# Performance work log

Hardware: AMD Instinct MI355X
Metric: run time of the kernel (lower is better)

The kernel has to match this reference:

```python
import jax, jax.numpy as jnp
import numpy as np

MAX_WAVELENGTH = 10000
BIG_NEG = -2.3819763e38


def _apply_rope(x, positions):
    """RoPE: positions [B,L] applied to x [B,L,H,D]."""
    d = x.shape[-1]
    freq_exponents = (2.0 / d) * jnp.arange(d // 2, dtype=jnp.float32)
    timescale = MAX_WAVELENGTH ** freq_exponents  # [D/2]
    radians = positions[..., None].astype(jnp.float32) / timescale  # [B,L,D/2]
    radians = radians[..., None, :]  # [B,L,1,D/2]
    sin, cos = jnp.sin(radians), jnp.cos(radians)
    x1, x2 = jnp.split(x, 2, axis=-1)
    return jnp.concatenate([x1 * cos - x2 * sin, x2 * cos + x1 * sin], axis=-1)


def setup_inputs() -> dict:
    key = jax.random.key(0)
    B, S, D, N, K, H = 2, 2048, 2048, 8, 1, 256  # batch, seq, features, q heads, kv heads, head_dim
    k1, k2, k3, k4 = jax.random.split(key, 4)
    x = jax.random.normal(k1, (B, S, D), dtype=jnp.float32)
    positions = jnp.broadcast_to(jnp.arange(S, dtype=jnp.int32), (B, S))
    attn_mask = jnp.tril(jnp.ones((S, S), dtype=bool))[None, None].repeat(B, axis=0)  # causal [B,1,S,S]
    q_w = jax.random.normal(k2, (N, D, H), dtype=jnp.float32) * (D ** -0.5)      # lecun_normal in_axis=-2
    kv_w = jax.random.normal(k3, (2, K, D, H), dtype=jnp.float32) * (D ** -0.5)
    out_w = jax.random.normal(k4, (N, H, D), dtype=jnp.float32) * (H ** -0.5)
    return {"x": x, "positions": positions, "attn_mask": attn_mask,
            "q_w": q_w, "kv_w": kv_w, "out_w": out_w}


def reference(x, positions, attn_mask, q_w, kv_w, out_w):
    B, T, D = x.shape
    N, _, H = q_w.shape
    K = kv_w.shape[1]
    G = N // K
    dtype = x.dtype

    q = jnp.einsum('btd,ndh->btnh', x, q_w)          # [B,T,N,H]
    kv = jnp.einsum('bsd,ckdh->cbskh', x, kv_w)      # [2,B,S,K,H]
    k, v = kv[0], kv[1]

    q = _apply_rope(q, positions) * (H ** -0.5)
    k = _apply_rope(k, positions)

    # prefill path: cache_size == S, so cache == k, v; idx = S
    qg = q.reshape(B, T, K, G, H)
    logits = jnp.einsum('btkgh,bskh->bkgts', qg, k,
                        preferred_element_type=jnp.float32)  # [B,K,G,T,S] fp32
    masked = jnp.where(attn_mask[:, :, None, :, :], logits, BIG_NEG)
    probs = jax.nn.softmax(masked, axis=-1).astype(dtype)
    enc = jnp.einsum('bkgts,bskh->btkgh', probs, v).reshape(B, T, N, H)
    out = jnp.einsum('btnh,nhd->btd', enc, out_w)
    return out
```

## Files before the change

### kernel.cpp

```cpp
#include <hip/hip_runtime.h>
#include <hip/hip_bf16.h>
#include <stdint.h>

#define BB 2
#define SS 2048
#define DD 2048
#define NHEAD 8
#define HH 256

typedef __bf16 bf16_t;
typedef __bf16 bf16x8 __attribute__((ext_vector_type(8)));
typedef __bf16 bf16x4v __attribute__((ext_vector_type(4)));
typedef __bf16 bf16x2v __attribute__((ext_vector_type(2)));
typedef float f32x4 __attribute__((ext_vector_type(4)));
typedef float f32x16 __attribute__((ext_vector_type(16)));
typedef unsigned int u32;

__device__ static inline void gload_lds16(const void* g, void* l) {
  __builtin_amdgcn_global_load_lds(
      (__attribute__((address_space(1))) void*)(g),
      (__attribute__((address_space(3))) void*)(l), 16, 0, 0);
}

__device__ static inline u32 pk2(float a, float b) {
  bf16x2v t = {(bf16_t)a, (bf16_t)b};
  return __builtin_bit_cast(u32, t);
}

__global__ void cvt_x_kernel(const float* __restrict__ x, bf16_t* __restrict__ xb) {
  size_t i = ((size_t)blockIdx.x * 256 + threadIdx.x) * 4;
  float4 v = *(const float4*)(x + i);
  bf16x4v o = {(bf16_t)v.x, (bf16_t)v.y, (bf16_t)v.z, (bf16_t)v.w};
  *(bf16x4v*)(xb + i) = o;
}

__global__ void transpose_cvt(const float* __restrict__ in, bf16_t* __restrict__ out,
                              int R, int C) {
  __shared__ float tile[32][33];
  int bx = blockIdx.x, by = blockIdx.y, z = blockIdx.z;
  in  += (size_t)z * R * C;
  out += (size_t)z * R * C;
  int tx = threadIdx.x & 31, ty = threadIdx.x >> 5;
#pragma unroll
  for (int k = 0; k < 4; ++k) {
    int r = by * 32 + ty + k * 8, c = bx * 32 + tx;
    tile[ty + k * 8][tx] = in[(size_t)r * C + c];
  }
  __syncthreads();
#pragma unroll
  for (int k = 0; k < 4; ++k) {
    int c = bx * 32 + ty + k * 8, r = by * 32 + tx;
    out[(size_t)c * R + r] = (bf16_t)tile[tx][ty + k * 8];
  }
}

template <int OUT_F32>
__global__ __launch_bounds__(512) void gemm3p(const bf16_t* __restrict__ A,
                                              const bf16_t* __restrict__ BT,
                                              void* __restrict__ C,
                                              int M, int Nc, int Kd) {
  __shared__ __attribute__((aligned(16))) char LDS[147456];
  char* Abuf = LDS;
  char* Bbuf = LDS + 98304;
  const int ntiles = Nc >> 7;
  int nwg = gridDim.x;
  int bid = ((nwg & 7) == 0) ? ((blockIdx.x & 7) * (nwg >> 3) + (blockIdx.x >> 3))
                             : blockIdx.x;
  int mt = bid / ntiles, ntb = bid % ntiles;
  int t = threadIdx.x, lane = t & 63, w = t >> 6;
  int wm = w >> 1, wn = w & 1;
  int l15 = lane & 15, lg = lane >> 4;
  int srow = t >> 3;
  int scolb = ((t & 7) * 16) ^ ((srow & 7) << 4);
  const bf16_t* Asrc = A + (size_t)(mt * 256 + srow) * Kd + (scolb >> 1);
  const bf16_t* Bsrc = BT + (size_t)(ntb * 128 + srow) * Kd + (scolb >> 1);
  const int nkt = Kd >> 6;
  f32x4 acc[4][4] = {};

#define STAGE_TILE(kt_)                                                      \
  {                                                                          \
    int buf_ = (kt_) % 3;                                                    \
    char* Ad_ = Abuf + buf_ * 32768 + t * 16;                                \
    char* Bd_ = Bbuf + buf_ * 16384 + t * 16;                                \
    const bf16_t* As_ = Asrc + (kt_)*64;                                     \
    const bf16_t* Bs_ = Bsrc + (kt_)*64;                                     \
    gload_lds16(As_, Ad_);                                                   \
    gload_lds16(As_ + (size_t)64 * Kd, Ad_ + 8192);                          \
    gload_lds16(As_ + (size_t)128 * Kd, Ad_ + 16384);                        \
    gload_lds16(As_ + (size_t)192 * Kd, Ad_ + 24576);                        \
    gload_lds16(Bs_, Bd_);                                                   \
    gload_lds16(Bs_ + (size_t)64 * Kd, Bd_ + 8192);                          \
  }

  STAGE_TILE(0);
  STAGE_TILE(1);
  asm volatile("s_waitcnt vmcnt(6)" ::: "memory");
  __builtin_amdgcn_s_barrier();
  asm volatile("" ::: "memory");
  for (int kt = 0; kt < nkt; ++kt) {
    if (kt + 2 < nkt) STAGE_TILE(kt + 2);
    const char* Ab = Abuf + (kt % 3) * 32768;
    const char* Bb = Bbuf + (kt % 3) * 16384;
    int swz = (l15 & 7) << 4;
#pragma unroll
    for (int ks = 0; ks < 2; ++ks) {
      bf16x8 af[4], bfr[4];
#pragma unroll
      for (int i = 0; i < 4; ++i)
        af[i] = *(const bf16x8*)(Ab + (wm * 64 + i * 16 + l15) * 128 +
                                 ((ks * 64 + lg * 16) ^ swz));
#pragma unroll
      for (int j = 0; j < 4; ++j)
        bfr[j] = *(const bf16x8*)(Bb + (wn * 64 + j * 16 + l15) * 128 +
                                  ((ks * 64 + lg * 16) ^ swz));
      __builtin_amdgcn_s_setprio(1);
#pragma unroll
      for (int i = 0; i < 4; ++i)
#pragma unroll
        for (int j = 0; j < 4; ++j)
          acc[i][j] = __builtin_amdgcn_mfma_f32_16x16x32_bf16(af[i], bfr[j], acc[i][j], 0, 0, 0);
      __builtin_amdgcn_s_setprio(0);
    }
    if (kt + 1 < nkt) {
      if (kt + 2 < nkt) {
        asm volatile("s_waitcnt vmcnt(6)" ::: "memory");
      } else {
        asm volatile("s_waitcnt vmcnt(0)" ::: "memory");
      }
      __builtin_amdgcn_s_barrier();
      asm volatile("" ::: "memory");
    }
  }
#undef STAGE_TILE
#pragma unroll
  for (int i = 0; i < 4; ++i)
#pragma unroll
    for (int j = 0; j < 4; ++j) {
      int row = mt * 256 + wm * 64 + i * 16 + lg * 4;
      int col = ntb * 128 + wn * 64 + j * 16 + l15;
#pragma unroll
      for (int v = 0; v < 4; ++v) {
        if (OUT_F32)
          ((float*)C)[(size_t)(row + v) * Nc + col] = acc[i][j][v];
        else
          ((bf16_t*)C)[(size_t)(row + v) * Nc + col] = (bf16_t)acc[i][j][v];
      }
    }
}

__global__ void rope_kernel(bf16_t* __restrict__ qkv, const int* __restrict__ positions) {
  int idx = blockIdx.x * 256 + threadIdx.x;
  const int QP = 4096 * 8 * 128;
  int i, row;
  bf16_t *p1, *p2;
  float scl;
  if (idx < QP) {
    i = idx & 127;
    int nh = (idx >> 7) & 7;
    row = idx >> 10;
    p1 = qkv + (size_t)row * 2560 + nh * 256 + i;
    p2 = p1 + 128;
    scl = 0.0625f;
  } else {
    int kk = idx - QP;
    if (kk >= 4096 * 128) return;
    i = kk & 127;
    row = kk >> 7;
    p1 = qkv + (size_t)row * 2560 + 2048 + i;
    p2 = p1 + 128;
    scl = 1.0f;
  }
  float pos = (float)positions[row];
  float ang = pos * __expf(-(float)i * (9.2103403719761836f / 128.f));
  float s = sinf(ang), c = cosf(ang);
  float x1 = (float)*p1, x2 = (float)*p2;
  *p1 = (bf16_t)((x1 * c - x2 * s) * scl);
  *p2 = (bf16_t)((x2 * c + x1 * s) * scl);
}

__global__ void vt_kernel(const bf16_t* __restrict__ qkv, bf16_t* __restrict__ vt) {
  __shared__ bf16_t tile[32][34];
  int bx = blockIdx.x;
  int by = blockIdx.y;
  int b = blockIdx.z;
  int tx = threadIdx.x & 31, ty = threadIdx.x >> 5;
#pragma unroll
  for (int k = 0; k < 4; ++k) {
    int s = bx * 32 + ty + k * 8, h = by * 32 + tx;
    tile[ty + k * 8][tx] = qkv[((size_t)(b * SS + s)) * 2560 + 2304 + h];
  }
  __syncthreads();
#pragma unroll
  for (int k = 0; k < 4; ++k) {
    int h = by * 32 + ty + k * 8, s = bx * 32 + tx;
    vt[((size_t)(b * HH + h)) * 2048 + s] = tile[tx][ty + k * 8];
  }
}

__global__ __launch_bounds__(512)
void flash_kernel(const bf16_t* __restrict__ qkv, const bf16_t* __restrict__ vtg,
                  bf16_t* __restrict__ enc, u32* __restrict__ ctr) {
  __shared__ __attribute__((aligned(16))) char LDSRAW[149504];
  char* Kl = LDSRAW;
  char* Vl = LDSRAW + 65536;
  char* Pl = LDSRAW + 131072;
  float* pmxL = (float*)(LDSRAW + 147456);
  float* scaleL = (float*)(LDSRAW + 147968);
  float* lsumL = (float*)(LDSRAW + 148480);
  u32* slot = (u32*)(LDSRAW + 148992);
  int t = threadIdx.x, lane = t & 63, w = t >> 6;
  int l31 = lane & 31, h5 = lane >> 5;
  bool isQK = (w < 4);
  int wq = isQK ? (w & 1) : ((w - 4) & 1);
  int sh = (w >> 1) & 1;
  int hh = ((w - 4) >> 1) & 1;
  int rk0 = t >> 5;
  int cbk = ((t & 31) * 16) ^ ((rk0 & 15) << 4);
  int rv0 = t >> 3;
  int cbv = ((t & 7) * 16) ^ ((rv0 & 7) << 4);

  for (;;) {
    if (t == 0) *slot = atomicAdd(ctr, 1);
    __syncthreads();
    u32 ti = *slot;
    if (ti >= 512u) break;
    int qt = 31 - (int)(ti >> 4);
    int b = (int)(ti >> 3) & 1, n = (int)ti & 7;
    const bf16_t* kbase = qkv + (size_t)(b * SS) * 2560 + 2048;
    int qmin = qt * 64 + wq * 32;
    int q_g = qmin + l31;
    bf16x8 qf[16];
    if (isQK) {
      const bf16_t* qrow = qkv + ((size_t)(b * SS + q_g)) * 2560 + n * 256 + h5 * 8;
#pragma unroll
      for (int i = 0; i < 16; ++i) qf[i] = *(const bf16x8*)(qrow + i * 16);
    }
    f32x16 accO[4] = {};
    float m_r = -1e30f, l_r = 0.f;
#pragma unroll
    for (int r = 0; r < 4; ++r)
      gload_lds16(kbase + (size_t)(rk0 + 16 * r) * 2560 + (cbk >> 1), Kl + t * 16 + r * 8192);
    __syncthreads();
    for (int kt = 0; kt <= qt + 1; ++kt) {
      int cur = kt & 1, prv = cur ^ 1;
      if (kt <= qt) {
#pragma unroll
        for (int r = 0; r < 4; ++r)
          gload_lds16(vtg + ((size_t)(b * HH + rv0 + 64 * r)) * 2048 + kt * 64 + (cbv >> 1),
                      Vl + cur * 32768 + t * 16 + r * 8192);
      }
      if (kt < qt) {
#pragma unroll
        for (int r = 0; r < 4; ++r)
          gload_lds16(kbase + (size_t)((kt + 1) * 64 + rk0 + 16 * r) * 2560 + (cbk >> 1),
                      Kl + prv * 32768 + t * 16 + r * 8192);
      }
      bool qact = isQK && (kt <= qt);
      bool act = qact && (kt * 64 + sh * 32 <= qmin + 31);
      bool pact = (!isQK) && (kt >= 1);
      f32x16 sc = {};
      float pm = -1e30f;
      if (qact) {
        if (act) {
          const char* Kc = Kl + cur * 32768;
          int krow = sh * 32 + l31;
          int kswz = (l31 & 15) << 4;
          __builtin_amdgcn_s_setprio(1);
#pragma unroll
          for (int i = 0; i < 16; ++i) {
            bf16x8 kf = *(const bf16x8*)(Kc + krow * 512 + ((i * 32 + h5 * 16) ^ kswz));
            sc = __builtin_amdgcn_mfma_f32_32x32x16_bf16(kf, qf[i], sc, 0, 0, 0);
          }
          __builtin_amdgcn_s_setprio(0);
          int smin = kt * 64 + sh * 32;
          if (smin + 31 > qmin) {
#pragma unroll
            for (int r = 0; r < 16; ++r) {
              int s_g = smin + ((r & 3) + 8 * (r >> 2) + 4 * h5);
              if (s_g > q_g) sc[r] = -1e30f;
            }
          }
          pm = sc[0];
#pragma unroll
          for (int r = 1; r < 16; ++r) pm = fmaxf(pm, sc[r]);
          pm = fmaxf(pm, __shfl_xor(pm, 32));
        }
        if (h5 == 0) pmxL[(wq * 2 + sh) * 32 + l31] = pm;
      }
      if (pact) {
        float sfac = scaleL[prv * 64 + wq * 32 + l31];
        if (__any(sfac != 1.f)) {
          float rv[16];
#pragma unroll
          for (int r = 0; r < 16; ++r) rv[r] = __shfl(sfac, (r & 3) + 8 * (r >> 2) + 4 * h5);
#pragma unroll
          for (int ht = 0; ht < 4; ++ht)
#pragma unroll
            for (int r = 0; r < 16; ++r) accO[ht][r] *= rv[r];
        }
        const char* Pw = Pl + prv * 8192 + wq * 4096;
        const char* Vc = Vl + prv * 32768;
        int pswz = (l31 & 7) << 4;
        __builtin_amdgcn_s_setprio(1);
#pragma unroll
        for (int j = 0; j < 2; ++j) {
          bf16x8 pf = *(const bf16x8*)(Pw + l31 * 128 + ((j * 32 + h5 * 16) ^ pswz));
#pragma unroll
          for (int ht = 0; ht < 4; ++ht) {
            int vrow = hh * 128 + ht * 32 + l31;
            bf16x8 vf = *(const bf16x8*)(Vc + vrow * 128 + ((j * 32 + h5 * 16) ^ pswz));
            accO[ht] = __builtin_amdgcn_mfma_f32_32x32x16_bf16(pf, vf, accO[ht], 0, 0, 0);
          }
        }
        __builtin_amdgcn_s_setprio(0);
      }
      asm volatile("s_waitcnt lgkmcnt(0)" ::: "memory");
      __builtin_amdgcn_s_barrier();
      asm volatile("" ::: "memory");
      if (qact) {
        float pmS = fmaxf(pmxL[(wq * 2) * 32 + l31], pmxL[(wq * 2 + 1) * 32 + l31]);
        float rsc = 1.f;
        if (pmS > m_r + 8.f) {
          rsc = __expf(m_r - pmS);
          m_r = pmS;
          l_r *= rsc;
        }
        if (sh == 0 && h5 == 0) scaleL[cur * 64 + wq * 32 + l31] = rsc;
        if (act) {
          float rs = 0.f;
#pragma unroll
          for (int r = 0; r < 16; ++r) {
            float p = __expf(sc[r] - m_r);
            sc[r] = p;
            rs += p;
          }
          rs += __shfl_xor(rs, 32);
          l_r += rs;
          u32 u0 = pk2(sc[0], sc[1]),  u1 = pk2(sc[2], sc[3]);
          u32 u2 = pk2(sc[4], sc[5]),  u3 = pk2(sc[6], sc[7]);
          u32 u4 = pk2(sc[8], sc[9]),  u5 = pk2(sc[10], sc[11]);
          u32 u6 = pk2(sc[12], sc[13]), u7 = pk2(sc[14], sc[15]);
          u32 x0 = __shfl_xor(u0, 32), x1 = __shfl_xor(u1, 32);
          u32 x2 = __shfl_xor(u2, 32), x3 = __shfl_xor(u3, 32);
          u32 x4 = __shfl_xor(u4, 32), x5 = __shfl_xor(u5, 32);
          u32 x6 = __shfl_xor(u6, 32), x7 = __shfl_xor(u7, 32);
          union { u32 wd[4]; bf16x8 v; } f0, f1;
          f0.wd[0] = h5 ? x2 : u0;  f0.wd[1] = h5 ? x3 : u1;
          f0.wd[2] = h5 ? u2 : x0;  f0.wd[3] = h5 ? u3 : x1;
          f1.wd[0] = h5 ? x6 : u4;  f1.wd[1] = h5 ? x7 : u5;
          f1.wd[2] = h5 ? u6 : x4;  f1.wd[3] = h5 ? u7 : x5;
          char* Pw = Pl + cur * 8192 + wq * 4096;
          int pswz = (l31 & 7) << 4;
          *(bf16x8*)(Pw + l31 * 128 + ((sh * 64 + h5 * 16) ^ pswz)) = f0.v;
          *(bf16x8*)(Pw + l31 * 128 + ((sh * 64 + 32 + h5 * 16) ^ pswz)) = f1.v;
        }
      }
      if (pact && ((kt - 1 < qt) || wq == 1)) {
        const char* Pw = Pl + prv * 8192 + wq * 4096;
        const char* Vc = Vl + prv * 32768;
        int pswz = (l31 & 7) << 4;
        __builtin_amdgcn_s_setprio(1);
#pragma unroll
        for (int j = 2; j < 4; ++j) {
          bf16x8 pf = *(const bf16x8*)(Pw + l31 * 128 + ((j * 32 + h5 * 16) ^ pswz));
#pragma unroll
          for (int ht = 0; ht < 4; ++ht) {
            int vrow = hh * 128 + ht * 32 + l31;
            bf16x8 vf = *(const bf16x8*)(Vc + vrow * 128 + ((j * 32 + h5 * 16) ^ pswz));
            accO[ht] = __builtin_amdgcn_mfma_f32_32x32x16_bf16(pf, vf, accO[ht], 0, 0, 0);
          }
        }
        __builtin_amdgcn_s_setprio(0);
      }
      __syncthreads();
    }
    if (isQK && h5 == 0) lsumL[sh * 64 + wq * 32 + l31] = l_r;
    __syncthreads();
    if (!isQK) {
      float lt = lsumL[wq * 32 + l31] + lsumL[64 + wq * 32 + l31];
      float rinv = 1.f / lt;
      float riv[16];
#pragma unroll
      for (int r = 0; r < 16; ++r) riv[r] = __shfl(rinv, (r & 3) + 8 * (r >> 2) + 4 * h5);
#pragma unroll
      for (int ht = 0; ht < 4; ++ht)
#pragma unroll
        for (int r = 0; r < 16; ++r) {
          int ql = (r & 3) + 8 * (r >> 2) + 4 * h5;
          enc[((size_t)(b * SS + qmin + ql)) * 2048 + n * 256 + hh * 128 + ht * 32 + l31] =
              (bf16_t)(accO[ht][r] * riv[r]);
        }
    }
  }
}

extern "C" void kernel_launch(void* const* d_in, const int* in_sizes, int n_in,
                              void* d_out, int out_size, void* d_ws, size_t ws_size,
                              hipStream_t stream) {
  const float* x = (const float*)d_in[0];
  const int* positions = (const int*)d_in[1];
  const float* qw = (const float*)d_in[3];
  const float* kvw = (const float*)d_in[4];
  const float* outw = (const float*)d_in[5];

  char* ws = (char*)d_ws;
  if (ws_size < (size_t)75497472) return;
  bf16_t* xb      = (bf16_t*)(ws);
  bf16_t* qkvwbt  = (bf16_t*)(ws + 16777216);
  bf16_t* outwbt  = (bf16_t*)(ws + 27262976);
  bf16_t* qkvb    = (bf16_t*)(ws + 35651584);
  bf16_t* vtg     = (bf16_t*)(ws + 56623104);
  bf16_t* encb    = (bf16_t*)(ws + 58720256);
  u32* ctr        = (u32*)(ws);

  cvt_x_kernel<<<8192, 256, 0, stream>>>(x, xb);
  transpose_cvt<<<dim3(8, 64, 8), 256, 0, stream>>>(qw, qkvwbt, 2048, 256);
  transpose_cvt<<<dim3(8, 64, 2), 256, 0, stream>>>(kvw, qkvwbt + (size_t)2048 * 2048, 2048, 256);
  transpose_cvt<<<dim3(64, 64, 1), 256, 0, stream>>>(outw, outwbt, 2048, 2048);
  gemm3p<0><<<320, 512, 0, stream>>>(xb, qkvwbt, qkvb, 4096, 2560, 2048);
  rope_kernel<<<18432, 256, 0, stream>>>(qkvb, positions);
  vt_kernel<<<dim3(64, 8, 2), 256, 0, stream>>>(qkvb, vtg);
  hipMemsetAsync(ctr, 0, 4, stream);
  flash_kernel<<<256, 512, 0, stream>>>(qkvb, vtg, encb, ctr);
  gemm3p<1><<<256, 512, 0, stream>>>(encb, outwbt, d_out, 4096, 2048, 2048);
}
```

Before: 209.0 us.

## Shrink GEMM tiles to 128x128 with 256 threads and split A/B staging

Replaces the 256x128 tile, 512-thread GEMM with a 128x128 tile using 256 threads (4 waves), doubling the grid size for both projection GEMMs. A is triple-buffered while B is double-buffered, and B is staged only one tile ahead, which cuts LDS use from 144KB to 80KB. The goal is more workgroups for better CU occupancy and load balance. The cost is lower per-block data reuse and more global traffic, and B now has less prefetch lead time.

```diff
diff --git a/kernel.cpp b/kernel.cpp
--- a/kernel.cpp
+++ b/kernel.cpp
@@ -55,13 +55,13 @@
 }
 
 template <int OUT_F32>
-__global__ __launch_bounds__(512) void gemm3p(const bf16_t* __restrict__ A,
+__global__ __launch_bounds__(256) void gemm2b(const bf16_t* __restrict__ A,
                                               const bf16_t* __restrict__ BT,
                                               void* __restrict__ C,
                                               int M, int Nc, int Kd) {
-  __shared__ __attribute__((aligned(16))) char LDS[147456];
+  __shared__ __attribute__((aligned(16))) char LDS[81920];
   char* Abuf = LDS;
-  char* Bbuf = LDS + 98304;
+  char* Bbuf = LDS + 49152;
   const int ntiles = Nc >> 7;
   int nwg = gridDim.x;
   int bid = ((nwg & 7) == 0) ? ((blockIdx.x & 7) * (nwg >> 3) + (blockIdx.x >> 3))
@@ -72,35 +72,41 @@
   int l15 = lane & 15, lg = lane >> 4;
   int srow = t >> 3;
   int scolb = ((t & 7) * 16) ^ ((srow & 7) << 4);
-  const bf16_t* Asrc = A + (size_t)(mt * 256 + srow) * Kd + (scolb >> 1);
+  const bf16_t* Asrc = A + (size_t)(mt * 128 + srow) * Kd + (scolb >> 1);
   const bf16_t* Bsrc = BT + (size_t)(ntb * 128 + srow) * Kd + (scolb >> 1);
   const int nkt = Kd >> 6;
   f32x4 acc[4][4] = {};
 
-#define STAGE_TILE(kt_)                                                      \
-  {                                                                          \
-    int buf_ = (kt_) % 3;                                                    \
-    char* Ad_ = Abuf + buf_ * 32768 + t * 16;                                \
-    char* Bd_ = Bbuf + buf_ * 16384 + t * 16;                                \
-    const bf16_t* As_ = Asrc + (kt_)*64;                                     \
-    const bf16_t* Bs_ = Bsrc + (kt_)*64;                                     \
-    gload_lds16(As_, Ad_);                                                   \
-    gload_lds16(As_ + (size_t)64 * Kd, Ad_ + 8192);                          \
-    gload_lds16(As_ + (size_t)128 * Kd, Ad_ + 16384);                        \
-    gload_lds16(As_ + (size_t)192 * Kd, Ad_ + 24576);                        \
-    gload_lds16(Bs_, Bd_);                                                   \
-    gload_lds16(Bs_ + (size_t)64 * Kd, Bd_ + 8192);                          \
-  }
-
-  STAGE_TILE(0);
-  STAGE_TILE(1);
-  asm volatile("s_waitcnt vmcnt(6)" ::: "memory");
+#define STAGE_A(kt_)                                                  \
+  {                                                                   \
+    char* d_ = Abuf + ((kt_) % 3) * 16384 + t * 16;                   \
+    const bf16_t* s_ = Asrc + (kt_)*64;                               \
+    gload_lds16(s_, d_);                                              \
+    gload_lds16(s_ + (size_t)32 * Kd, d_ + 4096);                     \
+    gload_lds16(s_ + (size_t)64 * Kd, d_ + 8192);                     \
+    gload_lds16(s_ + (size_t)96 * Kd, d_ + 12288);                    \
+  }
+#define STAGE_B(kt_)                                                  \
+  {                                                                   \
+    char* d_ = Bbuf + ((kt_)&1) * 16384 + t * 16;                     \
+    const bf16_t* s_ = Bsrc + (kt_)*64;                               \
+    gload_lds16(s_, d_);                                              \
+    gload_lds16(s_ + (size_t)32 * Kd, d_ + 4096);                     \
+    gload_lds16(s_ + (size_t)64 * Kd, d_ + 8192);                     \
+    gload_lds16(s_ + (size_t)96 * Kd, d_ + 12288);                    \
+  }
+
+  STAGE_A(0);
+  STAGE_B(0);
+  STAGE_A(1);
+  asm volatile("s_waitcnt vmcnt(4)" ::: "memory");
   __builtin_amdgcn_s_barrier();
   asm volatile("" ::: "memory");
   for (int kt = 0; kt < nkt; ++kt) {
-    if (kt + 2 < nkt) STAGE_TILE(kt + 2);
-    const char* Ab = Abuf + (kt % 3) * 32768;
-    const char* Bb = Bbuf + (kt % 3) * 16384;
+    if (kt + 1 < nkt) STAGE_B(kt + 1);
+    if (kt + 2 < nkt) STAGE_A(kt + 2);
+    const char* Ab = Abuf + (kt % 3) * 16384;
+    const char* Bb = Bbuf + (kt & 1) * 16384;
     int swz = (l15 & 7) << 4;
 #pragma unroll
     for (int ks = 0; ks < 2; ++ks) {
@@ -123,7 +129,7 @@
     }
     if (kt + 1 < nkt) {
       if (kt + 2 < nkt) {
-        asm volatile("s_waitcnt vmcnt(6)" ::: "memory");
+        asm volatile("s_waitcnt vmcnt(4)" ::: "memory");
       } else {
         asm volatile("s_waitcnt vmcnt(0)" ::: "memory");
       }
@@ -131,12 +137,13 @@
       asm volatile("" ::: "memory");
     }
   }
-#undef STAGE_TILE
+#undef STAGE_A
+#undef STAGE_B
 #pragma unroll
   for (int i = 0; i < 4; ++i)
 #pragma unroll
     for (int j = 0; j < 4; ++j) {
-      int row = mt * 256 + wm * 64 + i * 16 + lg * 4;
+      int row = mt * 128 + wm * 64 + i * 16 + lg * 4;
       int col = ntb * 128 + wn * 64 + j * 16 + l15;
 #pragma unroll
       for (int v = 0; v < 4; ++v) {
@@ -417,10 +424,10 @@
   transpose_cvt<<<dim3(8, 64, 8), 256, 0, stream>>>(qw, qkvwbt, 2048, 256);
   transpose_cvt<<<dim3(8, 64, 2), 256, 0, stream>>>(kvw, qkvwbt + (size_t)2048 * 2048, 2048, 256);
   transpose_cvt<<<dim3(64, 64, 1), 256, 0, stream>>>(outw, outwbt, 2048, 2048);
-  gemm3p<0><<<320, 512, 0, stream>>>(xb, qkvwbt, qkvb, 4096, 2560, 2048);
+  gemm2b<0><<<640, 256, 0, stream>>>(xb, qkvwbt, qkvb, 4096, 2560, 2048);
   rope_kernel<<<18432, 256, 0, stream>>>(qkvb, positions);
   vt_kernel<<<dim3(64, 8, 2), 256, 0, stream>>>(qkvb, vtg);
   hipMemsetAsync(ctr, 0, 4, stream);
   flash_kernel<<<256, 512, 0, stream>>>(qkvb, vtg, encb, ctr);
-  gemm3p<1><<<256, 512, 0, stream>>>(encb, outwbt, d_out, 4096, 2048, 2048);
-}
+  gemm2b<1><<<512, 256, 0, stream>>>(encb, outwbt, d_out, 4096, 2048, 2048);
+}
```

After: 200.7 us. 1.04x faster.
